# Kernel optimization log

Measured on AMD Instinct MI355X. Metric: run time of the kernel, lower is better.

Reference implementation:

```python
import jax, jax.numpy as jnp
import numpy as np

TINY = np.finfo(np.float32).tiny


def setup_inputs() -> dict:
    key = jax.random.key(0)
    k1, k2, k3 = jax.random.split(key, 3)
    B, IN, OUT = 4096, 4096, 1024
    x = jax.random.normal(k1, (B, IN), dtype=jnp.float32)
    weight = jax.random.normal(k2, (IN, OUT), dtype=jnp.float32)
    uniform = jax.random.uniform(k3, (IN, OUT), dtype=jnp.float32)
    T = jnp.ones((1,), dtype=jnp.float32)
    return {"x": x, "weight": weight, "uniform": uniform, "T": T}


def reference(x, weight, uniform, T):
    # training-path forward of ConcreteLayer
    # uniform -> (1 - tiny) * u + tiny, then Gumbel noise
    u = (1.0 - TINY) * uniform + TINY
    gumbel = -jnp.log(-jnp.log(u))                      # [in, out]
    noisy_logits = (weight + gumbel) / T                # temperature scaling
    samples = jax.nn.softmax(noisy_logits, axis=1)      # softmax over out dim (torch default for 2D)
    out = jnp.einsum('bi,ik->bk', x, samples)           # [batch, out]
    return out
```

## Files before the change

### kernel.cpp

```cpp
#include <hip/hip_runtime.h>
#include <cstdint>
#include <cstddef>


#define TINYF 1.17549435082228750797e-38f
#define LN2F 0.69314718055994530942f
#define LOG2EF 1.44269504088896340736f

typedef unsigned short u16;
typedef __attribute__((ext_vector_type(8))) short bf16x8;
typedef __attribute__((ext_vector_type(4))) float f32x4;

__device__ __forceinline__ u16 f2bf(float f) {
  union { float f; uint32_t u; } v; v.f = f;
  uint32_t r = v.u + 0x7FFFu + ((v.u >> 16) & 1u);
  return (u16)(r >> 16);
}

__device__ __forceinline__ float log2_hw(float x) { return __builtin_amdgcn_logf(x); }
__device__ __forceinline__ float exp2_hw(float x) { return __builtin_amdgcn_exp2f(x); }
__device__ __forceinline__ float rcp_hw(float x) { return __builtin_amdgcn_rcpf(x); }

__device__ __forceinline__ float gumbel_fast(float u) {
  float t = -log2_hw(u);
  return -LN2F * log2_hw(t * LN2F);
}
__device__ __forceinline__ float exp_fast(float x) { return exp2_hw(x * LOG2EF); }

__device__ __forceinline__ void gld_lds16(const void* g, void* l) {
  __builtin_amdgcn_global_load_lds(
      (__attribute__((address_space(1))) void*)(g),
      (__attribute__((address_space(3))) void*)(l), 16, 0, 0);
}

__global__ void trans_exp_kernel(const float* __restrict__ W, const float* __restrict__ U,
                                 const float* __restrict__ Tp, u16* __restrict__ BT,
                                 float* __restrict__ d, float4* __restrict__ out4) {
  __shared__ float tile[64][65];
  const int k0 = blockIdx.x * 64, n0 = blockIdx.y * 64;
  const int t = threadIdx.x;
  const float invT = 1.0f / Tp[0];

  {
    int bid = blockIdx.y * gridDim.x + blockIdx.x;
    float4 z = make_float4(0.f, 0.f, 0.f, 0.f);
#pragma unroll
    for (int j = 0; j < 4; ++j) out4[(size_t)bid * 1024 + j * 256 + t] = z;
  }

  {
    const int nn4 = (t & 15) * 4, kq = t >> 4;
#pragma unroll
    for (int r = 0; r < 4; ++r) {
      int kk = r * 16 + kq;
      size_t gi = (size_t)(k0 + kk) * 1024 + (n0 + nn4);
      float4 w = *(const float4*)&W[gi];
      float4 u = *(const float4*)&U[gi];
      float e0 = exp_fast((w.x + gumbel_fast(u.x * (1.0f - TINYF) + TINYF)) * invT);
      float e1 = exp_fast((w.y + gumbel_fast(u.y * (1.0f - TINYF) + TINYF)) * invT);
      float e2 = exp_fast((w.z + gumbel_fast(u.z * (1.0f - TINYF) + TINYF)) * invT);
      float e3 = exp_fast((w.w + gumbel_fast(u.w * (1.0f - TINYF) + TINYF)) * invT);
      tile[kk][nn4 + 0] = e0; tile[kk][nn4 + 1] = e1;
      tile[kk][nn4 + 2] = e2; tile[kk][nn4 + 3] = e3;
      float s = (e0 + e1) + (e2 + e3);
#pragma unroll
      for (int m = 8; m > 0; m >>= 1) s += __shfl_xor(s, m, 16);
      if ((t & 15) == 0) atomicAdd(&d[k0 + kk], s);
    }
  }
  __syncthreads();
  {
    const int kk4 = (t & 15) * 4, nq = t >> 4;
#pragma unroll
    for (int r = 0; r < 4; ++r) {
      int nn = r * 16 + nq;
      ushort4 o;
      o.x = f2bf(tile[kk4 + 0][nn]);
      o.y = f2bf(tile[kk4 + 1][nn]);
      o.z = f2bf(tile[kk4 + 2][nn]);
      o.w = f2bf(tile[kk4 + 3][nn]);
      *(ushort4*)&BT[(size_t)(n0 + nn) * 4096 + (k0 + kk4)] = o;
    }
  }
}

__global__ void cast_kernel(const float4* __restrict__ x, const float4* __restrict__ d4,
                            ushort4* __restrict__ xb, int n4x) {
  int i = blockIdx.x * blockDim.x + threadIdx.x;
  if (i >= n4x) return;
  int col4 = i & 1023;
  float4 v = x[i];
  float4 dd = d4[col4];
  ushort4 o;
  o.x = f2bf(v.x * rcp_hw(dd.x)); o.y = f2bf(v.y * rcp_hw(dd.y));
  o.z = f2bf(v.z * rcp_hw(dd.z)); o.w = f2bf(v.w * rcp_hw(dd.w));
  xb[i] = o;
}

#define TM 128
#define TN 128
#define TK 64
#define SPLITK 4

__launch_bounds__(256, 4)
__global__ void gemm_bt_kernel(const u16* __restrict__ A, const u16* __restrict__ BT,
                               float* __restrict__ C, int M, int N, int K) {
  __shared__ u16 As[TM * TK];
  __shared__ u16 Bs[TN * TK];

  const int tid = threadIdx.x;
  const int lane = tid & 63, w = tid >> 6;
  const int wm = w >> 1, wn = w & 1;
  const int m0 = blockIdx.x * TM, n0 = blockIdx.y * TN;
  const int quad = lane >> 4, r16 = lane & 15;
  const int srow = lane >> 3;
  const int sg = (lane & 7) ^ srow;

  const int kz = blockIdx.z;
  const int Kq = K / SPLITK;
  const u16* Ak = A + (size_t)kz * Kq;
  const u16* Bk = BT + (size_t)kz * Kq;

  f32x4 acc[4][4] = {};

  for (int kt = 0; kt < Kq; kt += TK) {
    __syncthreads();
#pragma unroll
    for (int c = 0; c < 4; ++c) {
      int chunk = w * 4 + c;
      gld_lds16(Ak + (size_t)(m0 + chunk * 8 + srow) * K + kt + sg * 8, (char*)As + chunk * 1024);
      gld_lds16(Bk + (size_t)(n0 + chunk * 8 + srow) * K + kt + sg * 8, (char*)Bs + chunk * 1024);
    }
    __syncthreads();

#pragma unroll
    for (int ss = 0; ss < 2; ++ss) {
      bf16x8 aF[4], bF[4];
#pragma unroll
      for (int mi = 0; mi < 4; ++mi) {
        int row = wm * 64 + mi * 16 + r16;
        aF[mi] = *(const bf16x8*)((const char*)As + row * 128 + (((ss * 4 + quad) ^ (row & 7)) * 16));
      }
#pragma unroll
      for (int ni = 0; ni < 4; ++ni) {
        int row = wn * 64 + ni * 16 + r16;
        bF[ni] = *(const bf16x8*)((const char*)Bs + row * 128 + (((ss * 4 + quad) ^ (row & 7)) * 16));
      }
#pragma unroll
      for (int mi = 0; mi < 4; ++mi)
#pragma unroll
        for (int ni = 0; ni < 4; ++ni)
          acc[mi][ni] = __builtin_amdgcn_mfma_f32_16x16x32_bf16(aF[mi], bF[ni], acc[mi][ni], 0, 0, 0);
    }
  }

#pragma unroll
  for (int mi = 0; mi < 4; ++mi)
#pragma unroll
    for (int ni = 0; ni < 4; ++ni)
#pragma unroll
      for (int r = 0; r < 4; ++r) {
        int row = m0 + wm * 64 + mi * 16 + quad * 4 + r;
        int col = n0 + wn * 64 + ni * 16 + r16;
        atomicAdd(&C[(size_t)row * N + col], acc[mi][ni][r]);
      }
}

extern "C" void kernel_launch(void* const* d_in, const int* in_sizes, int n_in,
                              void* d_out, int out_size, void* d_ws, size_t ws_size,
                              hipStream_t stream) {
  const int M = 4096, K = 4096, N = 1024;
  const float* x = (const float*)d_in[0];
  const float* W = (const float*)d_in[1];
  const float* U = (const float*)d_in[2];
  const float* Tp = (const float*)d_in[3];
  float* out = (float*)d_out;

  char* ws = (char*)d_ws;
  u16* xb = (u16*)ws;
  u16* bt = (u16*)(ws + (size_t)M * K * 2);
  float* dsum = (float*)(ws + (size_t)M * K * 2 + (size_t)N * K * 2);

  hipMemsetAsync(dsum, 0, K * sizeof(float), stream);
  trans_exp_kernel<<<dim3(K / 64, N / 64), 256, 0, stream>>>(W, U, Tp, bt, dsum, (float4*)out);
  cast_kernel<<<dim3(M * K / 4 / 256), 256, 0, stream>>>((const float4*)x, (const float4*)dsum,
                                                         (ushort4*)xb, M * K / 4);
  gemm_bt_kernel<<<dim3(M / TM, N / TN, SPLITK), 256, 0, stream>>>(xb, bt, out, M, N, K);
}
```

Before: 212.4 us.

## Fuse softmax prep, cast and GEMM into one persistent kernel with grid barriers

Replaces the three separate launches (exp/transpose, cast, split-K GEMM) with a single persistent 512-block kernel. Stages are separated by software grid barriers built on atomic counters. Split-K drops from 4 to 2, so the GEMM phase runs 512 tiles, one per block, with fewer atomic adds into the output. This removes per-launch overhead and inter-kernel gaps. In exchange, the GEMM runs on a fixed grid at lower occupancy, the barriers spin, and correctness relies on all 512 blocks being co-resident.

```diff
diff --git a/kernel.cpp b/kernel.cpp
--- a/kernel.cpp
+++ b/kernel.cpp
@@ -10,6 +10,8 @@
 typedef unsigned short u16;
 typedef __attribute__((ext_vector_type(8))) short bf16x8;
 typedef __attribute__((ext_vector_type(4))) float f32x4;
+
+#define NBLK 512
 
 __device__ __forceinline__ u16 f2bf(float f) {
   union { float f; uint32_t u; } v; v.f = f;
@@ -33,137 +35,165 @@
       (__attribute__((address_space(3))) void*)(l), 16, 0, 0);
 }
 
-__global__ void trans_exp_kernel(const float* __restrict__ W, const float* __restrict__ U,
-                                 const float* __restrict__ Tp, u16* __restrict__ BT,
-                                 float* __restrict__ d, float4* __restrict__ out4) {
-  __shared__ float tile[64][65];
-  const int k0 = blockIdx.x * 64, n0 = blockIdx.y * 64;
-  const int t = threadIdx.x;
-  const float invT = 1.0f / Tp[0];
-
-  {
-    int bid = blockIdx.y * gridDim.x + blockIdx.x;
-    float4 z = make_float4(0.f, 0.f, 0.f, 0.f);
-#pragma unroll
-    for (int j = 0; j < 4; ++j) out4[(size_t)bid * 1024 + j * 256 + t] = z;
-  }
-
-  {
-    const int nn4 = (t & 15) * 4, kq = t >> 4;
-#pragma unroll
-    for (int r = 0; r < 4; ++r) {
-      int kk = r * 16 + kq;
-      size_t gi = (size_t)(k0 + kk) * 1024 + (n0 + nn4);
-      float4 w = *(const float4*)&W[gi];
-      float4 u = *(const float4*)&U[gi];
-      float e0 = exp_fast((w.x + gumbel_fast(u.x * (1.0f - TINYF) + TINYF)) * invT);
-      float e1 = exp_fast((w.y + gumbel_fast(u.y * (1.0f - TINYF) + TINYF)) * invT);
-      float e2 = exp_fast((w.z + gumbel_fast(u.z * (1.0f - TINYF) + TINYF)) * invT);
-      float e3 = exp_fast((w.w + gumbel_fast(u.w * (1.0f - TINYF) + TINYF)) * invT);
-      tile[kk][nn4 + 0] = e0; tile[kk][nn4 + 1] = e1;
-      tile[kk][nn4 + 2] = e2; tile[kk][nn4 + 3] = e3;
-      float s = (e0 + e1) + (e2 + e3);
-#pragma unroll
-      for (int m = 8; m > 0; m >>= 1) s += __shfl_xor(s, m, 16);
-      if ((t & 15) == 0) atomicAdd(&d[k0 + kk], s);
-    }
-  }
+__device__ __forceinline__ void grid_barrier(unsigned* counter) {
   __syncthreads();
-  {
-    const int kk4 = (t & 15) * 4, nq = t >> 4;
-#pragma unroll
-    for (int r = 0; r < 4; ++r) {
-      int nn = r * 16 + nq;
-      ushort4 o;
-      o.x = f2bf(tile[kk4 + 0][nn]);
-      o.y = f2bf(tile[kk4 + 1][nn]);
-      o.z = f2bf(tile[kk4 + 2][nn]);
-      o.w = f2bf(tile[kk4 + 3][nn]);
-      *(ushort4*)&BT[(size_t)(n0 + nn) * 4096 + (k0 + kk4)] = o;
-    }
-  }
-}
-
-__global__ void cast_kernel(const float4* __restrict__ x, const float4* __restrict__ d4,
-                            ushort4* __restrict__ xb, int n4x) {
-  int i = blockIdx.x * blockDim.x + threadIdx.x;
-  if (i >= n4x) return;
-  int col4 = i & 1023;
-  float4 v = x[i];
-  float4 dd = d4[col4];
-  ushort4 o;
-  o.x = f2bf(v.x * rcp_hw(dd.x)); o.y = f2bf(v.y * rcp_hw(dd.y));
-  o.z = f2bf(v.z * rcp_hw(dd.z)); o.w = f2bf(v.w * rcp_hw(dd.w));
-  xb[i] = o;
+  if (threadIdx.x == 0) {
+    __threadfence();
+    __hip_atomic_fetch_add(counter, 1u, __ATOMIC_ACQ_REL, __HIP_MEMORY_SCOPE_AGENT);
+    while (__hip_atomic_load(counter, __ATOMIC_ACQUIRE, __HIP_MEMORY_SCOPE_AGENT) < NBLK)
+      __builtin_amdgcn_s_sleep(8);
+  }
+  __syncthreads();
+  __threadfence();
 }
 
 #define TM 128
 #define TN 128
 #define TK 64
-#define SPLITK 4
-
-__launch_bounds__(256, 4)
-__global__ void gemm_bt_kernel(const u16* __restrict__ A, const u16* __restrict__ BT,
-                               float* __restrict__ C, int M, int N, int K) {
-  __shared__ u16 As[TM * TK];
-  __shared__ u16 Bs[TN * TK];
-
-  const int tid = threadIdx.x;
-  const int lane = tid & 63, w = tid >> 6;
-  const int wm = w >> 1, wn = w & 1;
-  const int m0 = blockIdx.x * TM, n0 = blockIdx.y * TN;
-  const int quad = lane >> 4, r16 = lane & 15;
-  const int srow = lane >> 3;
-  const int sg = (lane & 7) ^ srow;
-
-  const int kz = blockIdx.z;
-  const int Kq = K / SPLITK;
-  const u16* Ak = A + (size_t)kz * Kq;
-  const u16* Bk = BT + (size_t)kz * Kq;
-
-  f32x4 acc[4][4] = {};
-
-  for (int kt = 0; kt < Kq; kt += TK) {
-    __syncthreads();
-#pragma unroll
-    for (int c = 0; c < 4; ++c) {
-      int chunk = w * 4 + c;
-      gld_lds16(Ak + (size_t)(m0 + chunk * 8 + srow) * K + kt + sg * 8, (char*)As + chunk * 1024);
-      gld_lds16(Bk + (size_t)(n0 + chunk * 8 + srow) * K + kt + sg * 8, (char*)Bs + chunk * 1024);
-    }
-    __syncthreads();
-
-#pragma unroll
-    for (int ss = 0; ss < 2; ++ss) {
-      bf16x8 aF[4], bF[4];
-#pragma unroll
-      for (int mi = 0; mi < 4; ++mi) {
-        int row = wm * 64 + mi * 16 + r16;
-        aF[mi] = *(const bf16x8*)((const char*)As + row * 128 + (((ss * 4 + quad) ^ (row & 7)) * 16));
-      }
-#pragma unroll
-      for (int ni = 0; ni < 4; ++ni) {
-        int row = wn * 64 + ni * 16 + r16;
-        bF[ni] = *(const bf16x8*)((const char*)Bs + row * 128 + (((ss * 4 + quad) ^ (row & 7)) * 16));
-      }
-#pragma unroll
-      for (int mi = 0; mi < 4; ++mi)
-#pragma unroll
-        for (int ni = 0; ni < 4; ++ni)
-          acc[mi][ni] = __builtin_amdgcn_mfma_f32_16x16x32_bf16(aF[mi], bF[ni], acc[mi][ni], 0, 0, 0);
-    }
-  }
-
-#pragma unroll
-  for (int mi = 0; mi < 4; ++mi)
-#pragma unroll
-    for (int ni = 0; ni < 4; ++ni)
-#pragma unroll
-      for (int r = 0; r < 4; ++r) {
-        int row = m0 + wm * 64 + mi * 16 + quad * 4 + r;
-        int col = n0 + wn * 64 + ni * 16 + r16;
-        atomicAdd(&C[(size_t)row * N + col], acc[mi][ni][r]);
-      }
+
+__launch_bounds__(256)
+__global__ void mega_kernel(const float* __restrict__ X, const float* __restrict__ W,
+                            const float* __restrict__ U, const float* __restrict__ Tp,
+                            u16* __restrict__ xb, u16* __restrict__ BT,
+                            float* __restrict__ dsum, unsigned* __restrict__ bar,
+                            float* __restrict__ C) {
+  __shared__ __align__(16) char smem[32768];
+  const int bid = blockIdx.x;
+  const int t = threadIdx.x;
+
+  {
+    float (*tile)[65] = (float(*)[65])smem;
+    const float invT = 1.0f / Tp[0];
+    {
+      float4 z = make_float4(0.f, 0.f, 0.f, 0.f);
+      float4* out4 = (float4*)C;
+#pragma unroll
+      for (int j = 0; j < 8; ++j) out4[(size_t)bid * 2048 + j * 256 + t] = z;
+    }
+#pragma unroll
+    for (int ti = 0; ti < 2; ++ti) {
+      int tix = bid * 2 + ti;
+      int k0 = (tix & 63) * 64, n0 = (tix >> 6) * 64;
+      __syncthreads();
+      {
+        const int nn4 = (t & 15) * 4, kq = t >> 4;
+#pragma unroll
+        for (int r = 0; r < 4; ++r) {
+          int kk = r * 16 + kq;
+          size_t gi = (size_t)(k0 + kk) * 1024 + (n0 + nn4);
+          float4 w = *(const float4*)&W[gi];
+          float4 u = *(const float4*)&U[gi];
+          float e0 = exp_fast((w.x + gumbel_fast(u.x * (1.0f - TINYF) + TINYF)) * invT);
+          float e1 = exp_fast((w.y + gumbel_fast(u.y * (1.0f - TINYF) + TINYF)) * invT);
+          float e2 = exp_fast((w.z + gumbel_fast(u.z * (1.0f - TINYF) + TINYF)) * invT);
+          float e3 = exp_fast((w.w + gumbel_fast(u.w * (1.0f - TINYF) + TINYF)) * invT);
+          tile[kk][nn4 + 0] = e0; tile[kk][nn4 + 1] = e1;
+          tile[kk][nn4 + 2] = e2; tile[kk][nn4 + 3] = e3;
+          float s = (e0 + e1) + (e2 + e3);
+#pragma unroll
+          for (int m = 8; m > 0; m >>= 1) s += __shfl_xor(s, m, 16);
+          if ((t & 15) == 0) atomicAdd(&dsum[k0 + kk], s);
+        }
+      }
+      __syncthreads();
+      {
+        const int kk4 = (t & 15) * 4, nq = t >> 4;
+#pragma unroll
+        for (int r = 0; r < 4; ++r) {
+          int nn = r * 16 + nq;
+          ushort4 o;
+          o.x = f2bf(tile[kk4 + 0][nn]);
+          o.y = f2bf(tile[kk4 + 1][nn]);
+          o.z = f2bf(tile[kk4 + 2][nn]);
+          o.w = f2bf(tile[kk4 + 3][nn]);
+          *(ushort4*)&BT[(size_t)(n0 + nn) * 4096 + (k0 + kk4)] = o;
+        }
+      }
+    }
+  }
+
+  grid_barrier(&bar[0]);
+
+  {
+    const float4* x4 = (const float4*)X;
+    const float4* d4 = (const float4*)dsum;
+    ushort4* xb4 = (ushort4*)xb;
+#pragma unroll
+    for (int j = 0; j < 32; ++j) {
+      int i = bid * 8192 + j * 256 + t;
+      int col4 = i & 1023;
+      float4 v = x4[i];
+      float4 dd = d4[col4];
+      ushort4 o;
+      o.x = f2bf(v.x * rcp_hw(dd.x)); o.y = f2bf(v.y * rcp_hw(dd.y));
+      o.z = f2bf(v.z * rcp_hw(dd.z)); o.w = f2bf(v.w * rcp_hw(dd.w));
+      xb4[i] = o;
+    }
+  }
+
+  grid_barrier(&bar[1]);
+
+  {
+    u16* As = (u16*)smem;
+    u16* Bs = (u16*)(smem + 16384);
+
+    const int lane = t & 63, w = t >> 6;
+    const int wm = w >> 1, wn = w & 1;
+    const int m0 = ((bid >> 3) & 31) * TM;
+    const int n0 = (bid & 7) * TN;
+    const int kz = bid >> 8;
+    const int quad = lane >> 4, r16 = lane & 15;
+    const int srow = lane >> 3;
+    const int sg = (lane & 7) ^ srow;
+
+    const int Kh = 2048;
+    const u16* Ak = xb + (size_t)kz * Kh;
+    const u16* Bk = BT + (size_t)kz * Kh;
+
+    f32x4 acc[4][4] = {};
+
+    for (int kt = 0; kt < Kh; kt += TK) {
+      __syncthreads();
+#pragma unroll
+      for (int c = 0; c < 4; ++c) {
+        int chunk = w * 4 + c;
+        gld_lds16(Ak + (size_t)(m0 + chunk * 8 + srow) * 4096 + kt + sg * 8, smem + chunk * 1024);
+        gld_lds16(Bk + (size_t)(n0 + chunk * 8 + srow) * 4096 + kt + sg * 8, smem + 16384 + chunk * 1024);
+      }
+      __syncthreads();
+
+#pragma unroll
+      for (int ss = 0; ss < 2; ++ss) {
+        bf16x8 aF[4], bF[4];
+#pragma unroll
+        for (int mi = 0; mi < 4; ++mi) {
+          int row = wm * 64 + mi * 16 + r16;
+          aF[mi] = *(const bf16x8*)((const char*)As + row * 128 + (((ss * 4 + quad) ^ (row & 7)) * 16));
+        }
+#pragma unroll
+        for (int ni = 0; ni < 4; ++ni) {
+          int row = wn * 64 + ni * 16 + r16;
+          bF[ni] = *(const bf16x8*)((const char*)Bs + row * 128 + (((ss * 4 + quad) ^ (row & 7)) * 16));
+        }
+#pragma unroll
+        for (int mi = 0; mi < 4; ++mi)
+#pragma unroll
+          for (int ni = 0; ni < 4; ++ni)
+            acc[mi][ni] = __builtin_amdgcn_mfma_f32_16x16x32_bf16(aF[mi], bF[ni], acc[mi][ni], 0, 0, 0);
+      }
+    }
+
+#pragma unroll
+    for (int mi = 0; mi < 4; ++mi)
+#pragma unroll
+      for (int ni = 0; ni < 4; ++ni)
+#pragma unroll
+        for (int r = 0; r < 4; ++r) {
+          int row = m0 + wm * 64 + mi * 16 + quad * 4 + r;
+          int col = n0 + wn * 64 + ni * 16 + r16;
+          atomicAdd(&C[(size_t)row * 1024 + col], acc[mi][ni][r]);
+        }
+  }
 }
 
 extern "C" void kernel_launch(void* const* d_in, const int* in_sizes, int n_in,
@@ -180,10 +210,8 @@
   u16* xb = (u16*)ws;
   u16* bt = (u16*)(ws + (size_t)M * K * 2);
   float* dsum = (float*)(ws + (size_t)M * K * 2 + (size_t)N * K * 2);
-
-  hipMemsetAsync(dsum, 0, K * sizeof(float), stream);
-  trans_exp_kernel<<<dim3(K / 64, N / 64), 256, 0, stream>>>(W, U, Tp, bt, dsum, (float4*)out);
-  cast_kernel<<<dim3(M * K / 4 / 256), 256, 0, stream>>>((const float4*)x, (const float4*)dsum,
-                                                         (ushort4*)xb, M * K / 4);
-  gemm_bt_kernel<<<dim3(M / TM, N / TN, SPLITK), 256, 0, stream>>>(xb, bt, out, M, N, K);
-}
+  unsigned* bar = (unsigned*)(dsum + K);
+
+  hipMemsetAsync(dsum, 0, K * sizeof(float) + 2 * sizeof(unsigned), stream);
+  mega_kernel<<<dim3(NBLK), 256, 0, stream>>>(x, W, U, Tp, xb, bt, dsum, bar, out);
+}
```

After: 436.3 us. 2.05x slower.
